# Performance work log

Measured on AMD Instinct MI355X. Metric: run time of the kernel, lower is better.

## Reference

```python
import jax, jax.numpy as jnp
import numpy as np

EMBED_DIM = 1024
N_HEADS = 16
HEAD_DIM = EMBED_DIM // N_HEADS
BATCH = 2
SEQ = 2048


def setup_inputs() -> dict:
    key = jax.random.key(0)
    ks = jax.random.split(key, 12)
    s = 1.0 / np.sqrt(EMBED_DIM)
    return {
        "x": jax.random.normal(ks[0], (BATCH, SEQ, EMBED_DIM), jnp.float32),
        "q_w": jax.random.normal(ks[1], (EMBED_DIM, EMBED_DIM), jnp.float32) * s,
        "q_b": jax.random.normal(ks[2], (EMBED_DIM,), jnp.float32) * s,
        "k_w": jax.random.normal(ks[3], (EMBED_DIM, EMBED_DIM), jnp.float32) * s,
        "k_b": jax.random.normal(ks[4], (EMBED_DIM,), jnp.float32) * s,
        "v_w": jax.random.normal(ks[5], (EMBED_DIM, EMBED_DIM), jnp.float32) * s,
        "v_b": jax.random.normal(ks[6], (EMBED_DIM,), jnp.float32) * s,
        "phase": jax.random.normal(ks[7], (N_HEADS, HEAD_DIM), jnp.float32),
        "entanglement": jax.random.normal(ks[8], (N_HEADS, HEAD_DIM, HEAD_DIM), jnp.float32) * 0.1,
        "out_w": jax.random.normal(ks[9], (EMBED_DIM, EMBED_DIM), jnp.float32) * s,
        "out_b": jax.random.normal(ks[10], (EMBED_DIM,), jnp.float32) * s,
    }


def reference(x, q_w, q_b, k_w, k_b, v_w, v_b, phase, entanglement, out_w, out_b):
    b, s, _ = x.shape
    # projections -> [b, h, s, d]
    def split_heads(y):
        return y.reshape(b, s, N_HEADS, HEAD_DIM).transpose(0, 2, 1, 3)
    Q = split_heads(x @ q_w + q_b)
    K = split_heads(x @ k_w + k_b)
    V = split_heads(x @ v_w + v_b)
    # real part of phase-rotated Q/K: Q * cos(phase) (imag discarded by .real)
    cosp = jnp.cos(phase)[None, :, None, :]  # [1, h, 1, d]
    Qc = Q * cosp
    Kc = K * cosp
    scores = jnp.einsum('bhqd,bhkd->bhqk', Qc, Kc) / np.sqrt(HEAD_DIM)
    # bilinear entanglement term: Q . E . K^T per head
    scores = scores + jnp.einsum('bhqd,hde,bhke->bhqk', Q, entanglement, K)
    attn = jax.nn.softmax(scores, axis=-1)
    attended = jnp.einsum('bhqk,bhkd->bhqd', attn, V)
    attended = attended.transpose(0, 2, 1, 3).reshape(b, s, EMBED_DIM)
    return attended @ out_w + out_b
```

## Files before the change

kernel.cpp:

```cpp
#include <hip/hip_runtime.h>
#include <hip/hip_bf16.h>

typedef __bf16 bf16;
typedef __bf16 bf16x8 __attribute__((ext_vector_type(8)));
typedef __bf16 bf16x4 __attribute__((ext_vector_type(4)));
typedef float f32x4 __attribute__((ext_vector_type(4)));
typedef float f32x16 __attribute__((ext_vector_type(16)));
typedef unsigned int u32x2 __attribute__((ext_vector_type(2)));

#define EMBED 1024
#define NH 16
#define HD 64
#define BATCH 2
#define SEQ 2048
#define MTOK 4096
#define LOG2E 1.4426950408889634f

static __device__ __forceinline__ float fast_exp2(float x) {
#if __has_builtin(__builtin_amdgcn_exp2f)
  return __builtin_amdgcn_exp2f(x);
#else
  float r;
  asm("v_exp_f32 %0, %1" : "=v"(r) : "v"(x));
  return r;
#endif
}

static __device__ __forceinline__ f32x4 mfma16(bf16x8 a, bf16x8 b, f32x4 c) {
  return __builtin_amdgcn_mfma_f32_16x16x32_bf16(a, b, c, 0, 0, 0);
}
static __device__ __forceinline__ f32x16 mfma32(bf16x8 a, bf16x8 b, f32x16 c) {
  return __builtin_amdgcn_mfma_f32_32x32x16_bf16(a, b, c, 0, 0, 0);
}

static __device__ __forceinline__ void gld_lds16(const bf16* g, bf16* l) {
  __builtin_amdgcn_global_load_lds(
      (const __attribute__((address_space(1))) void*)g,
      (__attribute__((address_space(3))) void*)l, 16, 0, 0);
}

__global__ __launch_bounds__(256) void prep_kernel(
    const float* __restrict__ x, const float* __restrict__ qw,
    const float* __restrict__ qb, const float* __restrict__ kw,
    const float* __restrict__ vw, const float* __restrict__ ow,
    const float* __restrict__ ent, const float* __restrict__ phase,
    bf16* __restrict__ xb, bf16* __restrict__ wtall, bf16* __restrict__ wot,
    float* __restrict__ beff) {
  __shared__ float t0[64][65];
  __shared__ float t1[64][65];
  const int bb = blockIdx.x;
  const int tid = threadIdx.x;

  if (bb < 2048) {
    const int n4 = MTOK * EMBED / 4;
    int i = bb * 256 + tid;
    for (; i < n4; i += 2048 * 256) {
      f32x4 v = ((const f32x4*)x)[i];
      bf16x4 o;
      o[0] = (bf16)v[0]; o[1] = (bf16)v[1]; o[2] = (bf16)v[2]; o[3] = (bf16)v[3];
      ((bf16x4*)xb)[i] = o;
    }
    return;
  }
  if (bb < 2816) {
    const int idx = (bb - 2048) & 255;
    const float* W = (bb < 2304) ? kw : (bb < 2560) ? vw : ow;
    bf16* Wt = (bb < 2304) ? (wtall + 1024 * 1024)
             : (bb < 2560) ? (wtall + 2 * 1024 * 1024) : wot;
    const int bc = (idx & 15) * 64;
    const int br = (idx >> 4) * 64;
#pragma unroll
    for (int j = 0; j < 16; j++) {
      int id2 = j * 256 + tid;
      int r = id2 >> 6, c = id2 & 63;
      t0[r][c] = W[(size_t)(br + r) * EMBED + bc + c];
    }
    __syncthreads();
#pragma unroll
    for (int j = 0; j < 16; j++) {
      int id2 = j * 256 + tid;
      int r = id2 >> 6, c = id2 & 63;
      Wt[(size_t)(bc + r) * EMBED + br + c] = (bf16)t0[c][r];
    }
    return;
  }
  if (bb < 3072) {
    const int idx = bb - 2816;
    const int h = idx >> 4;
    const int ibase = (idx & 15) * 64;
#pragma unroll
    for (int j = 0; j < 16; j++) {
      int id2 = j * 256 + tid;
      int i = id2 >> 6, d = id2 & 63;
      t0[i][d] = qw[(size_t)(ibase + i) * EMBED + h * HD + d];
    }
#pragma unroll
    for (int j = 0; j < 16; j++) {
      int id2 = j * 256 + tid;
      int d = id2 >> 6, e = id2 & 63;
      float v = ent[((size_t)h * HD + d) * HD + e];
      if (d == e) { float cp = cosf(phase[h * HD + d]); v += cp * cp * 0.125f; }
      t1[d][e] = v * LOG2E;
    }
    __syncthreads();
    const int i = tid & 63;
    const int e0 = (tid >> 6) * 16;
    float s[16];
#pragma unroll
    for (int ee = 0; ee < 16; ee++) s[ee] = 0.f;
    for (int d = 0; d < 64; d++) {
      float qv = t0[i][d];
#pragma unroll
      for (int ee = 0; ee < 16; ee++) s[ee] += qv * t1[d][e0 + ee];
    }
#pragma unroll
    for (int ee = 0; ee < 16; ee++)
      wtall[(size_t)(h * HD + e0 + ee) * EMBED + ibase + i] = (bf16)s[ee];
    return;
  }
  const int h = bb - 3072;
  if (tid < 64) {
    const int e = tid;
    float s = 0.f;
    for (int d = 0; d < 64; d++) {
      float v = ent[((size_t)h * HD + d) * HD + e];
      if (d == e) { float cp = cosf(phase[h * HD + d]); v += cp * cp * 0.125f; }
      s += qb[h * HD + d] * v;
    }
    beff[h * HD + e] = s * LOG2E;
  }
}

template <int EPI>
__global__ __launch_bounds__(256) void gemm_bt_kernel(
    const bf16* __restrict__ A, const bf16* __restrict__ Bt,
    const float* __restrict__ bias_q, const float* __restrict__ bias_k,
    const float* __restrict__ bias_v, const float* __restrict__ bias_o,
    bf16* __restrict__ Qp, bf16* __restrict__ Kp, bf16* __restrict__ Vt,
    float* __restrict__ Fout) {
  const int tid = threadIdx.x;
  const int lane = tid & 63, w = tid >> 6;
  const int g = lane >> 4, r15 = lane & 15;
  const int wr = w >> 1, wc = w & 1;
  const int bm = blockIdx.x * 128;
  const int bn = blockIdx.y * 128;

  __shared__ bf16 sA[128 * 32];
  __shared__ bf16 sB[128 * 32];

  f32x4 acc[4][4];
#pragma unroll
  for (int m = 0; m < 4; m++)
#pragma unroll
    for (int n = 0; n < 4; n++) acc[m][n] = (f32x4){0.f, 0.f, 0.f, 0.f};

  const int srow = tid >> 2;
  const int scol = (tid & 3) << 3;
  const bf16* aptr = A + (size_t)(bm + srow) * EMBED + scol;
  const bf16* bptr = Bt + (size_t)(bn + srow) * EMBED + scol;
  bf16* la = sA + tid * 8;
  bf16* lb = sB + tid * 8;

  for (int k0 = 0; k0 < EMBED; k0 += 32) {
    __syncthreads();
    gld_lds16(aptr + k0, la);
    gld_lds16(aptr + k0 + 64 * EMBED, la + 64 * 32);
    gld_lds16(bptr + k0, lb);
    gld_lds16(bptr + k0 + 64 * EMBED, lb + 64 * 32);
    __syncthreads();
    bf16x8 af[4], bfv[4];
#pragma unroll
    for (int m = 0; m < 4; m++)
      af[m] = *(const bf16x8*)&sA[(wr * 64 + m * 16 + r15) * 32 + g * 8];
#pragma unroll
    for (int n = 0; n < 4; n++)
      bfv[n] = *(const bf16x8*)&sB[(wc * 64 + n * 16 + r15) * 32 + g * 8];
#pragma unroll
    for (int m = 0; m < 4; m++)
#pragma unroll
      for (int n = 0; n < 4; n++) acc[m][n] = mfma16(af[m], bfv[n], acc[m][n]);
  }

  const int orow0 = bm + wr * 64;
  if (EPI == 0) {
    const int seg = bn >> 10;
    const int clb = (bn & 1023) + wc * 64;
#pragma unroll
    for (int n = 0; n < 4; n++) {
      const int cl = clb + n * 16 + r15;
      const float bias = (seg == 0) ? bias_q[cl] : (seg == 1) ? bias_k[cl] : bias_v[cl];
#pragma unroll
      for (int m = 0; m < 4; m++) {
        const int row0 = orow0 + m * 16 + g * 4;
        if (seg == 2) {
          const int b = row0 >> 11, s = row0 & 2047;
          const int hh = cl >> 6, d = cl & 63;
          bf16x4 pk;
#pragma unroll
          for (int r = 0; r < 4; r++) pk[r] = (bf16)(acc[m][n][r] + bias);
          *(bf16x4*)(Vt + ((size_t)((b * NH + hh) * HD + d)) * SEQ + s) = pk;
        } else {
          bf16* dst = ((seg == 0) ? Qp : Kp) + (size_t)row0 * EMBED + cl;
#pragma unroll
          for (int r = 0; r < 4; r++) dst[(size_t)r * EMBED] = (bf16)(acc[m][n][r] + bias);
        }
      }
    }
  } else {
    const int ocol0 = bn + wc * 64;
#pragma unroll
    for (int n = 0; n < 4; n++) {
      const int col = ocol0 + n * 16 + r15;
      const float bias = bias_o[col];
#pragma unroll
      for (int m = 0; m < 4; m++) {
        const int row0 = orow0 + m * 16 + g * 4;
#pragma unroll
        for (int r = 0; r < 4; r++)
          Fout[(size_t)(row0 + r) * EMBED + col] = acc[m][n][r] + bias;
      }
    }
  }
}

__global__ __launch_bounds__(512, 4) void flash_attn_kernel(
    const bf16* __restrict__ Qp, const bf16* __restrict__ Kp,
    const bf16* __restrict__ Vt, bf16* __restrict__ Op) {
  const int tid = threadIdx.x, lane = tid & 63, w = tid >> 6;
  const int q31 = lane & 31, hi = lane >> 5;
  const int half = w >> 2, wq = w & 3;
  const int flat = blockIdx.x;
  const int c = (flat & 7) * 64 + (flat >> 3);
  const int bh = c >> 4, qt = c & 15;
  const int b = bh >> 4, h = bh & 15;

  __shared__ char smem[65536];
  bf16* sKb = (bf16*)smem;
  bf16* sVb = (bf16*)(smem + 32768);

  const int g256 = tid & 255;
  const int strow = g256 >> 3;
  const int stcb = (g256 & 7) << 4;

  const char* kgbase = (const char*)(Kp + ((size_t)b * SEQ) * EMBED + h * HD);
  const char* vgbase = (const char*)(Vt + (size_t)bh * HD * SEQ);

  auto stage = [&](int buf, int kv0) {
    bf16* kd = sKb + (size_t)(half * 2 + buf) * 4096 + g256 * 8;
    bf16* vd = sVb + (size_t)(half * 2 + buf) * 4096 + g256 * 8;
#pragma unroll
    for (int i = 0; i < 2; i++) {
      const int row = i * 32 + strow;
      const int sb = stcb ^ ((row & 7) << 4);
      gld_lds16((const bf16*)(kgbase + (size_t)(kv0 + row) * (EMBED * 2) + sb),
                kd + i * 2048);
      gld_lds16((const bf16*)(vgbase + (size_t)row * (SEQ * 2) + (size_t)kv0 * 2 + sb),
                vd + i * 2048);
    }
  };

  const int kvbase = half * 1024;
  stage(0, kvbase);

  const int qbase = qt * 128 + wq * 32;
  const int qrow = qbase + q31;
  const bf16* qptr = Qp + ((size_t)(b * SEQ + qrow)) * EMBED + h * HD;
  bf16x8 aq[4];
#pragma unroll
  for (int ds = 0; ds < 4; ds++)
    aq[ds] = *(const bf16x8*)(qptr + ds * 16 + hi * 8);

  const int sz = (q31 & 7) << 4;
  int cofs[4];
#pragma unroll
  for (int i = 0; i < 4; i++) cofs[i] = ((i * 32 + hi * 16) ^ sz);

  f32x16 o0, o1;
#pragma unroll
  for (int i = 0; i < 16; i++) { o0[i] = 0.f; o1[i] = 0.f; }
  float mrow = -3.0e38f, lrow = 0.f;

  union B4 { bf16x4 v; unsigned int u[2]; };

  for (int it = 0; it < 16; ++it) {
    const int cur = it & 1;
    if (it + 1 < 16) {
      stage(cur ^ 1, kvbase + (it + 1) * 64);
      asm volatile("s_waitcnt vmcnt(4)" ::: "memory");
    } else {
      asm volatile("s_waitcnt vmcnt(0)" ::: "memory");
    }
    __builtin_amdgcn_s_barrier();

    const char* kc = (const char*)(sKb + (size_t)(half * 2 + cur) * 4096) + q31 * 128;
    const char* vc = (const char*)(sVb + (size_t)(half * 2 + cur) * 4096) + q31 * 128;

    f32x16 s0, s1;
#pragma unroll
    for (int i = 0; i < 16; i++) { s0[i] = 0.f; s1[i] = 0.f; }
    __builtin_amdgcn_s_setprio(1);
#pragma unroll
    for (int ds = 0; ds < 4; ds++) {
      bf16x8 bk0 = *(const bf16x8*)(kc + cofs[ds]);
      bf16x8 bk1 = *(const bf16x8*)(kc + 4096 + cofs[ds]);
      s0 = mfma32(bk0, aq[ds], s0);
      s1 = mfma32(bk1, aq[ds], s1);
    }
    __builtin_amdgcn_s_setprio(0);

    float mt = s0[0];
#pragma unroll
    for (int i = 1; i < 16; i++) mt = fmaxf(mt, s0[i]);
#pragma unroll
    for (int i = 0; i < 16; i++) mt = fmaxf(mt, s1[i]);
    {
      u32x2 sm = __builtin_amdgcn_permlane32_swap(__float_as_uint(mt),
                                                  __float_as_uint(mt), false, false);
      mt = fmaxf(__uint_as_float(sm.x), __uint_as_float(sm.y));
    }
    if (__any(mt > mrow + 8.f)) {
      const float mn = fmaxf(mrow, mt);
      const float al = fast_exp2(mrow - mn);
      mrow = mn;
      lrow *= al;
      o0 *= al;
      o1 *= al;
    }

    B4 qd[8];
    float lsum = 0.f;
#pragma unroll
    for (int j = 0; j < 4; j++)
#pragma unroll
      for (int r = 0; r < 4; r++) {
        float pv = fast_exp2(s0[4 * j + r] - mrow);
        lsum += pv;
        qd[j].v[r] = (bf16)pv;
      }
#pragma unroll
    for (int j = 0; j < 4; j++)
#pragma unroll
      for (int r = 0; r < 4; r++) {
        float pv = fast_exp2(s1[4 * j + r] - mrow);
        lsum += pv;
        qd[4 + j].v[r] = (bf16)pv;
      }
    {
      u32x2 ss = __builtin_amdgcn_permlane32_swap(__float_as_uint(lsum),
                                                  __float_as_uint(lsum), false, false);
      lrow += __uint_as_float(ss.x) + __uint_as_float(ss.y);
    }

    bf16x8 pfrag[4];
#pragma unroll
    for (int kt = 0; kt < 4; kt++) {
      u32x2 p0 = __builtin_amdgcn_permlane32_swap(qd[2 * kt].u[0],
                                                  qd[2 * kt + 1].u[0], false, false);
      u32x2 p1 = __builtin_amdgcn_permlane32_swap(qd[2 * kt].u[1],
                                                  qd[2 * kt + 1].u[1], false, false);
      union { unsigned int u[4]; bf16x8 v; } f;
      f.u[0] = p0.x; f.u[1] = p1.x; f.u[2] = p0.y; f.u[3] = p1.y;
      pfrag[kt] = f.v;
    }

    __builtin_amdgcn_s_setprio(1);
#pragma unroll
    for (int kt = 0; kt < 4; kt++) {
      bf16x8 av0 = *(const bf16x8*)(vc + cofs[kt]);
      bf16x8 av1 = *(const bf16x8*)(vc + 4096 + cofs[kt]);
      o0 = mfma32(av0, pfrag[kt], o0);
      o1 = mfma32(av1, pfrag[kt], o1);
    }
    __builtin_amdgcn_s_setprio(0);
    __builtin_amdgcn_s_barrier();
  }

  float* shO = (float*)smem;
  float* shML = (float*)(smem + 33792);
  if (half == 1) {
    float* o = shO + (size_t)(wq * 64 + lane) * 33;
#pragma unroll
    for (int i = 0; i < 16; i++) { o[i] = o0[i]; o[16 + i] = o1[i]; }
    shML[(wq * 64 + lane) * 2] = mrow;
    shML[(wq * 64 + lane) * 2 + 1] = lrow;
  }
  __syncthreads();
  if (half == 0) {
    const float* o = shO + (size_t)(wq * 64 + lane) * 33;
    const float mB = shML[(wq * 64 + lane) * 2];
    const float lB = shML[(wq * 64 + lane) * 2 + 1];
    const float M = fmaxf(mrow, mB);
    const float wA = fast_exp2(mrow - M), wB = fast_exp2(mB - M);
    const float inv = 1.f / (lrow * wA + lB * wB);
    const float fA = wA * inv, fB = wB * inv;

    bf16* obase = Op + ((size_t)(b * SEQ + qrow)) * EMBED + h * HD;
#pragma unroll
    for (int j = 0; j < 4; j++) {
      bf16x4 st;
#pragma unroll
      for (int r = 0; r < 4; r++)
        st[r] = (bf16)(o0[4 * j + r] * fA + o[4 * j + r] * fB);
      *(bf16x4*)(obase + 8 * j + 4 * hi) = st;
    }
#pragma unroll
    for (int j = 0; j < 4; j++) {
      bf16x4 st;
#pragma unroll
      for (int r = 0; r < 4; r++)
        st[r] = (bf16)(o1[4 * j + r] * fA + o[16 + 4 * j + r] * fB);
      *(bf16x4*)(obase + 32 + 8 * j + 4 * hi) = st;
    }
  }
}

extern "C" void kernel_launch(void* const* d_in, const int* in_sizes, int n_in,
                              void* d_out, int out_size, void* d_ws, size_t ws_size,
                              hipStream_t stream) {
  const float* x     = (const float*)d_in[0];
  const float* q_w   = (const float*)d_in[1];
  const float* q_b   = (const float*)d_in[2];
  const float* k_w   = (const float*)d_in[3];
  const float* k_b   = (const float*)d_in[4];
  const float* v_w   = (const float*)d_in[5];
  const float* v_b   = (const float*)d_in[6];
  const float* phase = (const float*)d_in[7];
  const float* ent   = (const float*)d_in[8];
  const float* out_w = (const float*)d_in[9];
  const float* out_b = (const float*)d_in[10];
  float* out = (float*)d_out;

  char* ws = (char*)d_ws;
  bf16* xb    = (bf16*)(ws + 0);
  bf16* wtall = (bf16*)(ws + 8388608);
  bf16* wot   = (bf16*)(ws + 14680064);
  float* beff = (float*)(ws + 16777216);
  bf16* Qp    = (bf16*)(ws + 16781312);
  bf16* Kp    = (bf16*)(ws + 25169920);
  bf16* Vt    = (bf16*)(ws + 33558528);
  (void)in_sizes; (void)n_in; (void)out_size; (void)ws_size;

  prep_kernel<<<3088, 256, 0, stream>>>(x, q_w, q_b, k_w, v_w, out_w, ent, phase,
                                        xb, wtall, wot, beff);

  gemm_bt_kernel<0><<<dim3(32, 24), 256, 0, stream>>>(
      xb, wtall, beff, k_b, v_b, nullptr, Qp, Kp, Vt, nullptr);

  flash_attn_kernel<<<512, 512, 0, stream>>>(Qp, Kp, Vt, xb);

  gemm_bt_kernel<1><<<dim3(32, 8), 256, 0, stream>>>(
      xb, wot, nullptr, nullptr, nullptr, out_b, nullptr, nullptr, nullptr, out);
}
```

Before: 137.4 us.

## Transpose MFMA operands for vectorized Q/K/out stores, split V GEMM, swizzle blocks

For the Q/K projection and the output GEMM, the MFMA operands are swapped so that each lane holds four consecutive columns. This lets the epilogue issue 8-byte bf16x4 or 16-byte float4 row stores and vector bias loads instead of strided scalar stores. The V projection moves to its own launch that keeps the transposed Vt store path. A block-index swizzle is added to improve L2 locality. The cost is one extra kernel launch.

```diff
diff --git a/kernel.cpp b/kernel.cpp
--- a/kernel.cpp
+++ b/kernel.cpp
@@ -131,19 +131,21 @@
   }
 }
 
-template <int EPI>
+template <int MODE>
 __global__ __launch_bounds__(256) void gemm_bt_kernel(
     const bf16* __restrict__ A, const bf16* __restrict__ Bt,
-    const float* __restrict__ bias_q, const float* __restrict__ bias_k,
-    const float* __restrict__ bias_v, const float* __restrict__ bias_o,
-    bf16* __restrict__ Qp, bf16* __restrict__ Kp, bf16* __restrict__ Vt,
-    float* __restrict__ Fout) {
+    const float* __restrict__ bias0, const float* __restrict__ bias1,
+    bf16* __restrict__ O0, bf16* __restrict__ O1, float* __restrict__ FO) {
   const int tid = threadIdx.x;
   const int lane = tid & 63, w = tid >> 6;
   const int g = lane >> 4, r15 = lane & 15;
   const int wr = w >> 1, wc = w & 1;
-  const int bm = blockIdx.x * 128;
-  const int bn = blockIdx.y * 128;
+
+  const int flat = blockIdx.y * gridDim.x + blockIdx.x;
+  const int nwg = gridDim.x * gridDim.y;
+  const int swz = (flat & 7) * (nwg >> 3) + (flat >> 3);
+  const int bm = (swz & 31) * 128;
+  const int bn = (swz >> 5) * 128;
 
   __shared__ bf16 sA[128 * 32];
   __shared__ bf16 sB[128 * 32];
@@ -175,49 +177,65 @@
 #pragma unroll
     for (int n = 0; n < 4; n++)
       bfv[n] = *(const bf16x8*)&sB[(wc * 64 + n * 16 + r15) * 32 + g * 8];
-#pragma unroll
-    for (int m = 0; m < 4; m++)
-#pragma unroll
-      for (int n = 0; n < 4; n++) acc[m][n] = mfma16(af[m], bfv[n], acc[m][n]);
-  }
-
-  const int orow0 = bm + wr * 64;
-  if (EPI == 0) {
+    if (MODE == 1) {
+#pragma unroll
+      for (int m = 0; m < 4; m++)
+#pragma unroll
+        for (int n = 0; n < 4; n++) acc[m][n] = mfma16(af[m], bfv[n], acc[m][n]);
+    } else {
+#pragma unroll
+      for (int m = 0; m < 4; m++)
+#pragma unroll
+        for (int n = 0; n < 4; n++) acc[m][n] = mfma16(bfv[n], af[m], acc[m][n]);
+    }
+  }
+
+  if (MODE == 0) {
     const int seg = bn >> 10;
+    const float* bias = seg ? bias1 : bias0;
+    bf16* dst = seg ? O1 : O0;
     const int clb = (bn & 1023) + wc * 64;
+#pragma unroll
+    for (int n = 0; n < 4; n++) {
+      const int cl4 = clb + n * 16 + g * 4;
+      const f32x4 b4 = *(const f32x4*)&bias[cl4];
+#pragma unroll
+      for (int m = 0; m < 4; m++) {
+        const int tr = bm + wr * 64 + m * 16 + r15;
+        bf16x4 pk;
+#pragma unroll
+        for (int r = 0; r < 4; r++) pk[r] = (bf16)(acc[m][n][r] + b4[r]);
+        *(bf16x4*)(dst + (size_t)tr * EMBED + cl4) = pk;
+      }
+    }
+  } else if (MODE == 1) {
+    const int clb = bn + wc * 64;
+    const int orow0 = bm + wr * 64;
 #pragma unroll
     for (int n = 0; n < 4; n++) {
       const int cl = clb + n * 16 + r15;
-      const float bias = (seg == 0) ? bias_q[cl] : (seg == 1) ? bias_k[cl] : bias_v[cl];
+      const float bias = bias0[cl];
+      const int hh = cl >> 6, d = cl & 63;
 #pragma unroll
       for (int m = 0; m < 4; m++) {
         const int row0 = orow0 + m * 16 + g * 4;
-        if (seg == 2) {
-          const int b = row0 >> 11, s = row0 & 2047;
-          const int hh = cl >> 6, d = cl & 63;
-          bf16x4 pk;
-#pragma unroll
-          for (int r = 0; r < 4; r++) pk[r] = (bf16)(acc[m][n][r] + bias);
-          *(bf16x4*)(Vt + ((size_t)((b * NH + hh) * HD + d)) * SEQ + s) = pk;
-        } else {
-          bf16* dst = ((seg == 0) ? Qp : Kp) + (size_t)row0 * EMBED + cl;
-#pragma unroll
-          for (int r = 0; r < 4; r++) dst[(size_t)r * EMBED] = (bf16)(acc[m][n][r] + bias);
-        }
+        const int b = row0 >> 11, s = row0 & 2047;
+        bf16x4 pk;
+#pragma unroll
+        for (int r = 0; r < 4; r++) pk[r] = (bf16)(acc[m][n][r] + bias);
+        *(bf16x4*)(O0 + ((size_t)((b * NH + hh) * HD + d)) * SEQ + s) = pk;
       }
     }
   } else {
-    const int ocol0 = bn + wc * 64;
+    const int clb = bn + wc * 64;
 #pragma unroll
     for (int n = 0; n < 4; n++) {
-      const int col = ocol0 + n * 16 + r15;
-      const float bias = bias_o[col];
+      const int cl4 = clb + n * 16 + g * 4;
+      const f32x4 b4 = *(const f32x4*)&bias0[cl4];
 #pragma unroll
       for (int m = 0; m < 4; m++) {
-        const int row0 = orow0 + m * 16 + g * 4;
-#pragma unroll
-        for (int r = 0; r < 4; r++)
-          Fout[(size_t)(row0 + r) * EMBED + col] = acc[m][n][r] + bias;
+        const int tr = bm + wr * 64 + m * 16 + r15;
+        *(f32x4*)(FO + (size_t)tr * EMBED + cl4) = acc[m][n] + b4;
       }
     }
   }
@@ -443,11 +461,13 @@
   prep_kernel<<<3088, 256, 0, stream>>>(x, q_w, q_b, k_w, v_w, out_w, ent, phase,
                                         xb, wtall, wot, beff);
 
-  gemm_bt_kernel<0><<<dim3(32, 24), 256, 0, stream>>>(
-      xb, wtall, beff, k_b, v_b, nullptr, Qp, Kp, Vt, nullptr);
+  gemm_bt_kernel<0><<<dim3(32, 16), 256, 0, stream>>>(
+      xb, wtall, beff, k_b, Qp, Kp, nullptr);
+  gemm_bt_kernel<1><<<dim3(32, 8), 256, 0, stream>>>(
+      xb, wtall + 2 * 1024 * 1024, v_b, nullptr, Vt, nullptr, nullptr);
 
   flash_attn_kernel<<<512, 512, 0, stream>>>(Qp, Kp, Vt, xb);
 
-  gemm_bt_kernel<1><<<dim3(32, 8), 256, 0, stream>>>(
-      xb, wot, nullptr, nullptr, nullptr, out_b, nullptr, nullptr, nullptr, out);
-}
+  gemm_bt_kernel<2><<<dim3(32, 8), 256, 0, stream>>>(
+      xb, wot, out_b, nullptr, nullptr, nullptr, out);
+}
```

Result: slower. 162.2 us (+18.0%).
